# Performance work log

Measured on AMD Instinct MI355X. Metric: run time of the kernel, lower is better.

The kernel has to match this reference:

```python
import jax, jax.numpy as jnp
import numpy as np

B = 2
H = 256; Wd = 256; C = 128; S = 16        # image dims, channels, split_size
G = (H // S) * (Wd // S)                  # 256 heads (spatial groups)
N = S * S                                 # 256 patches per head
CI = C // 2                               # 64 channels per branch (gmlp input)
EI = 6                                    # inner gMLP expansion (MabGmlpBlock default e)
F1 = CI * EI                              # 384 = LocallyConnected expansion width
HF = F1 // 2                              # 192 = u/v split width
EPS = 1e-3                                # keras LayerNormalization default epsilon


def layer_norm(x, g, b):
    m = jnp.mean(x, axis=-1, keepdims=True)
    v = jnp.var(x, axis=-1, keepdims=True)
    return (x - m) * jax.lax.rsqrt(v + EPS) * g + b


def make_blocks(x):
    # 'B (H b1) (W b2) C -> B (H W) (b1 b2) C'
    b_, _, _, c_ = x.shape
    x = x.reshape(b_, H // S, S, Wd // S, S, c_)
    return x.transpose(0, 1, 3, 2, 4, 5).reshape(b_, G, N, c_)


def recon_blocks(x):
    # 'B (H W) (b1 b2) C -> B (H b1) (W b2) C'
    b_, _, _, c_ = x.shape
    x = x.reshape(b_, H // S, Wd // S, S, S, c_)
    return x.transpose(0, 1, 3, 2, 4, 5).reshape(b_, H, Wd, c_)


def recon_grids(x):
    # 'B (H W) (d1 d2) C -> B (d1 H) (d2 W) C'
    b_, _, _, c_ = x.shape
    x = x.reshape(b_, H // S, Wd // S, S, S, c_)
    return x.transpose(0, 3, 1, 4, 2, 5).reshape(b_, H, Wd, c_)


def gmlp(x, ln2_g, ln2_b, W1, b1, ln3_g, ln3_b, Wsgu, bsgu, W2, b2):
    # x: [B, G, N, CI]; all heads share weights -> batched einsum over (B, G)
    y = layer_norm(x, ln2_g, ln2_b)
    # LocallyConnected1D kernel_size=1: per-patch distinct weight [N, CI, F1]
    y = jax.nn.gelu(jnp.einsum('bgnc,ncf->bgnf', y, W1) + b1, approximate=False)
    u, v = jnp.split(y, 2, axis=-1)                      # [B,G,N,HF] each
    u = layer_norm(u, ln3_g, ln3_b)
    u = jnp.swapaxes(u, -1, -2)                          # [B,G,HF,N]
    # spatial gating: per-channel distinct [N->N] mixing, bias init ones
    u = jnp.einsum('bgcn,cnm->bgcm', u, Wsgu) + bsgu
    u = jnp.swapaxes(u, -1, -2)                          # [B,G,N,HF]
    return jnp.einsum('bgnc,ncf->bgnf', u * v, W2) + b2 + x


def setup_inputs() -> dict:
    key = jax.random.key(0)
    ks = jax.random.split(key, 8)
    x = jax.random.normal(ks[0], (B, H, Wd, C), jnp.float32)
    W_proj = jax.random.normal(ks[1], (C, C), jnp.float32) / np.sqrt(C).astype(np.float32)
    b_proj = jnp.zeros((C,), jnp.float32)
    W1 = jax.random.normal(ks[2], (N, CI, F1), jnp.float32) / np.sqrt(CI).astype(np.float32)
    b1 = jnp.zeros((N, F1), jnp.float32)
    Wsgu = jax.random.normal(ks[3], (HF, N, N), jnp.float32) * 0.001  # truncated_normal(0.001) approx
    bsgu = jnp.ones((HF, N), jnp.float32)                             # bias_initializer=ones
    W2 = jax.random.normal(ks[4], (N, HF, CI), jnp.float32) / np.sqrt(HF).astype(np.float32)
    b2 = jnp.zeros((N, CI), jnp.float32)
    return {
        'x': x,
        'ln1_g': jnp.ones((C,), jnp.float32), 'ln1_b': jnp.zeros((C,), jnp.float32),
        'W_proj': W_proj, 'b_proj': b_proj,
        'ln2_g': jnp.ones((CI,), jnp.float32), 'ln2_b': jnp.zeros((CI,), jnp.float32),
        'W1': W1, 'b1': b1,
        'ln3_g': jnp.ones((HF,), jnp.float32), 'ln3_b': jnp.zeros((HF,), jnp.float32),
        'Wsgu': Wsgu, 'bsgu': bsgu,
        'W2': W2, 'b2': b2,
    }


def reference(x, ln1_g, ln1_b, W_proj, b_proj, ln2_g, ln2_b, W1, b1,
              ln3_g, ln3_b, Wsgu, bsgu, W2, b2):
    y = layer_norm(x, ln1_g, ln1_b)
    y = jax.nn.gelu(y @ W_proj + b_proj, approximate=False)   # Dense(c*e), e=1
    local, glob = jnp.split(y, 2, axis=-1)                    # [B,H,W,CI] each
    g_args = (ln2_g, ln2_b, W1, b1, ln3_g, ln3_b, Wsgu, bsgu, W2, b2)
    local = recon_grids(gmlp(make_blocks(local), *g_args))    # multi-axis: block in, grid out
    glob = recon_blocks(gmlp(make_blocks(glob), *g_args))
    out = jnp.concatenate([local, glob], axis=-1) + x
    return out, glob
```

## Files before the change

### kernel.cpp

```cpp
#include <hip/hip_runtime.h>


typedef unsigned int uint_t;
typedef unsigned short us_t;
typedef __attribute__((ext_vector_type(8))) short bf16x8;
typedef __attribute__((ext_vector_type(4))) float f32x4;

#define EPSF 1e-3f

__device__ __forceinline__ float b2f(us_t h){ return __uint_as_float(((uint_t)h) << 16); }
__device__ __forceinline__ float lo2f(uint_t u){ return __uint_as_float(u << 16); }
__device__ __forceinline__ float hi2f(uint_t u){ return __uint_as_float(u & 0xFFFF0000u); }
__device__ __forceinline__ us_t f2b(float f){
  uint_t u = __float_as_uint(f);
  uint_t r = (u + 0x7FFFu + ((u >> 16) & 1u)) >> 16;
  return (us_t)r;
}
__device__ __forceinline__ uint_t pack2(float a, float b){
  return (uint_t)f2b(a) | ((uint_t)f2b(b) << 16);
}
__device__ __forceinline__ float gelu_f(float v){
  return 0.5f*v*(1.f + erff(v*0.7071067811865475f));
}

__global__ __launch_bounds__(256) void wprep(const float* __restrict__ Wsgu,
                                             const float* __restrict__ Wp,
                                             us_t* __restrict__ WT,
                                             us_t* __restrict__ WpT){
  __shared__ __align__(16) us_t ls[128*136];
  int t = threadIdx.x;
  if (blockIdx.x == 768){
    #pragma unroll
    for (int i = 0; i < 16; i++){
      int idx = (i*256 + t)*4;
      int row = idx >> 7, col = idx & 127;
      float4 w = *(const float4*)(Wp + idx);
      ls[(col+0)*136 + row] = f2b(w.x);
      ls[(col+1)*136 + row] = f2b(w.y);
      ls[(col+2)*136 + row] = f2b(w.z);
      ls[(col+3)*136 + row] = f2b(w.w);
    }
    __syncthreads();
    #pragma unroll
    for (int i = 0; i < 8; i++){
      int chunk = i*256 + t;
      int o = chunk >> 4, i0 = (chunk & 15) << 3;
      *(uint4*)(WpT + o*128 + i0) = *(const uint4*)&ls[o*136 + i0];
    }
    return;
  }
  int c = blockIdx.x >> 2, kt = blockIdx.x & 3;
  const float* src = Wsgu + ((size_t)c*256 + kt*64)*256;
  #pragma unroll
  for (int i = 0; i < 16; i++){
    int chunk = i*256 + t;
    int kk = chunk >> 6, mm = (chunk & 63) << 2;
    float4 w = *(const float4*)(src + kk*256 + mm);
    *(uint2*)&ls[kk*264 + mm] = make_uint2(pack2(w.x,w.y), pack2(w.z,w.w));
  }
  __syncthreads();
  #pragma unroll
  for (int i = 0; i < 8; i++){
    int chunk = i*256 + t;
    int m = chunk >> 3, kk0 = (chunk & 7) << 3;
    const us_t* sp = &ls[kk0*264 + m];
    uint4 o;
    o.x = (uint_t)sp[0]     | ((uint_t)sp[264]   << 16);
    o.y = (uint_t)sp[2*264] | ((uint_t)sp[3*264] << 16);
    o.z = (uint_t)sp[4*264] | ((uint_t)sp[5*264] << 16);
    o.w = (uint_t)sp[6*264] | ((uint_t)sp[7*264] << 16);
    *(uint4*)(WT + ((size_t)c*256 + m)*256 + kt*64 + kk0) = o;
  }
}

__global__ __launch_bounds__(256) void k1_ln_proj(
    const float* __restrict__ x, const float* __restrict__ g1, const float* __restrict__ b1l,
    const us_t* __restrict__ WpT, const float* __restrict__ bp, us_t* __restrict__ xin)
{
  __shared__ __align__(16) us_t As[128*136];
  __shared__ __align__(16) us_t Ws[128*136];
  __shared__ float gs[128], bs[128];
  int t = threadIdx.x;
  int p0 = blockIdx.x * 128;
  int lane = t & 63, wv = t >> 6;

  if (t < 128){ gs[t] = g1[t]; bs[t] = b1l[t]; }
  #pragma unroll
  for (int i = 0; i < 8; i++){
    int chunk = i*256 + t;
    int row = chunk >> 4, k0 = (chunk & 15) << 3;
    *(uint4*)&Ws[row*136 + k0] = *(const uint4*)(WpT + row*128 + k0);
  }
  int pl = t >> 1, half = t & 1;
  const float* xr = x + (size_t)(p0 + pl)*128 + half*64;
  float xv[64];
  float s = 0.f, q = 0.f;
  #pragma unroll
  for (int i = 0; i < 16; i++){
    float4 d = *(const float4*)(xr + i*4);
    xv[i*4+0] = d.x; xv[i*4+1] = d.y; xv[i*4+2] = d.z; xv[i*4+3] = d.w;
    s += d.x + d.y + d.z + d.w;
    q += d.x*d.x + d.y*d.y + d.z*d.z + d.w*d.w;
  }
  s += __shfl_xor(s, 1, 64);
  q += __shfl_xor(q, 1, 64);
  float m = s*(1.f/128.f);
  float rstd = rsqrtf(q*(1.f/128.f) - m*m + EPSF);
  __syncthreads();
  {
    int c0 = half << 6;
    us_t* dst = &As[pl*136 + c0];
    #pragma unroll
    for (int jj = 0; jj < 8; jj++){
      float y[8];
      #pragma unroll
      for (int k = 0; k < 8; k++){
        int idx = jj*8 + k;
        y[k] = (xv[idx] - m)*rstd*gs[c0 + idx] + bs[c0 + idx];
      }
      uint4 o;
      o.x = pack2(y[0], y[1]);
      o.y = pack2(y[2], y[3]);
      o.z = pack2(y[4], y[5]);
      o.w = pack2(y[6], y[7]);
      *(uint4*)&dst[jj*8] = o;
    }
  }
  __syncthreads();
  int wm0 = (wv >> 1) * 64, wn0 = (wv & 1) * 64;
  int fr = lane & 15, fq = lane >> 4;
  f32x4 acc[4][4] = {};
  #pragma unroll
  for (int sstep = 0; sstep < 4; sstep++){
    int kb = sstep*32 + fq*8;
    bf16x8 a[4], b[4];
    #pragma unroll
    for (int mi = 0; mi < 4; mi++)
      a[mi] = *(const bf16x8*)&Ws[(wm0 + mi*16 + fr)*136 + kb];
    #pragma unroll
    for (int ni = 0; ni < 4; ni++)
      b[ni] = *(const bf16x8*)&As[(wn0 + ni*16 + fr)*136 + kb];
    #pragma unroll
    for (int mi = 0; mi < 4; mi++)
      #pragma unroll
      for (int ni = 0; ni < 4; ni++)
        acc[mi][ni] = __builtin_amdgcn_mfma_f32_16x16x32_bf16(a[mi], b[ni], acc[mi][ni], 0, 0, 0);
  }
  #pragma unroll
  for (int mi = 0; mi < 4; mi++){
    int ch0 = wm0 + mi*16 + fq*4;
    float4 bb = *(const float4*)(bp + ch0);
    int branch = ch0 >> 6, c = ch0 & 63;
    #pragma unroll
    for (int ni = 0; ni < 4; ni++){
      int p = p0 + wn0 + ni*16 + fr;
      int b_ = p >> 16, rem = p & 65535, h = rem >> 8, w = rem & 255;
      int g = ((h >> 4) << 4) | (w >> 4);
      int nn = ((h & 15) << 4) | (w & 15);
      float v0 = gelu_f(acc[mi][ni][0] + bb.x);
      float v1 = gelu_f(acc[mi][ni][1] + bb.y);
      float v2 = gelu_f(acc[mi][ni][2] + bb.z);
      float v3 = gelu_f(acc[mi][ni][3] + bb.w);
      size_t row = (size_t)branch*512 + (size_t)b_*256 + g;
      *(uint2*)(xin + (row*256 + nn)*64 + c) = make_uint2(pack2(v0,v1), pack2(v2,v3));
    }
  }
}

__global__ __launch_bounds__(256) void k2_e1(
    const us_t* __restrict__ xin,
    const float* __restrict__ g2, const float* __restrict__ b2l,
    const float* __restrict__ W1, const float* __restrict__ b1v,
    const float* __restrict__ g3, const float* __restrict__ b3l,
    us_t* __restrict__ u_ln, us_t* __restrict__ vout, int r_base)
{
  __shared__ __align__(16) us_t Wl[64*384];
  __shared__ __align__(16) float xs2[64*36];
  __shared__ float b1s[384];
  int t = threadIdx.x;
  int n = blockIdx.x >> 2, rt = blockIdx.x & 3;

  const float* wsrc = W1 + (size_t)n*24576;
  #pragma unroll
  for (int i = 0; i < 24; i++){
    int idx = (i*256 + t)*4;
    float4 w = *(const float4*)(wsrc + idx);
    *(uint2*)&Wl[idx] = make_uint2(pack2(w.x,w.y), pack2(w.z,w.w));
  }
  if (t < 96){
    float4 d = *(const float4*)(b1v + n*384 + t*4);
    b1s[t*4+0] = d.x; b1s[t*4+1] = d.y; b1s[t*4+2] = d.z; b1s[t*4+3] = d.w;
  }
  {
    int rr = t >> 3, cc0 = (t & 7) << 3;
    uint4 d = *(const uint4*)(xin + ((size_t)(r_base + rt*32 + rr)*256 + n)*64 + cc0);
    float* dst = &xs2[cc0*36 + rr];
    dst[0]    = lo2f(d.x); dst[36]   = hi2f(d.x);
    dst[2*36] = lo2f(d.y); dst[3*36] = hi2f(d.y);
    dst[4*36] = lo2f(d.z); dst[5*36] = hi2f(d.z);
    dst[6*36] = lo2f(d.w); dst[7*36] = hi2f(d.w);
  }
  __syncthreads();
  {
    int wv = t >> 6, ln = t & 63;
    float gch = g2[ln], bch = b2l[ln];
    for (int k = 0; k < 8; k++){
      int row = wv*8 + k;
      float a = xs2[ln*36 + row];
      float s = a, q = a*a;
      #pragma unroll
      for (int off = 32; off; off >>= 1){ s += __shfl_xor(s, off, 64); q += __shfl_xor(q, off, 64); }
      float m = s*(1.f/64.f);
      float rstd = rsqrtf(q*(1.f/64.f) - m*m + EPSF);
      xs2[ln*36 + row] = (a - m)*rstd*gch + bch;
    }
  }
  __syncthreads();
  int fg = t & 31, rg = t >> 5;
  int f0 = fg*12, r00 = rg*4;
  float acc[4][12] = {};
  #pragma unroll 4
  for (int ci = 0; ci < 64; ci++){
    float4 xv = *(const float4*)&xs2[ci*36 + r00];
    const uint2* wp2 = (const uint2*)&Wl[ci*384 + f0];
    uint2 wa = wp2[0], wb = wp2[1], wc = wp2[2];
    float wf[12];
    wf[0]=lo2f(wa.x); wf[1]=hi2f(wa.x); wf[2]=lo2f(wa.y); wf[3]=hi2f(wa.y);
    wf[4]=lo2f(wb.x); wf[5]=hi2f(wb.x); wf[6]=lo2f(wb.y); wf[7]=hi2f(wb.y);
    wf[8]=lo2f(wc.x); wf[9]=hi2f(wc.x); wf[10]=lo2f(wc.y); wf[11]=hi2f(wc.y);
    float xa[4] = {xv.x, xv.y, xv.z, xv.w};
    #pragma unroll
    for (int i = 0; i < 4; i++)
      #pragma unroll
      for (int j = 0; j < 12; j++)
        acc[i][j] += xa[i]*wf[j];
  }
  bool isu = (fg < 16);
  float s4[4], q4[4];
  #pragma unroll
  for (int i = 0; i < 4; i++){
    float s = 0.f, q = 0.f;
    #pragma unroll
    for (int j = 0; j < 12; j++){
      float yv = gelu_f(acc[i][j] + b1s[f0 + j]);
      acc[i][j] = yv;
      s += yv; q += yv*yv;
    }
    s4[i] = isu ? s : 0.f;
    q4[i] = isu ? q : 0.f;
  }
  #pragma unroll
  for (int i = 0; i < 4; i++){
    float s = s4[i], q = q4[i];
    #pragma unroll
    for (int off = 16; off; off >>= 1){ s += __shfl_xor(s, off, 64); q += __shfl_xor(q, off, 64); }
    float m = s*(1.f/192.f);
    s4[i] = m;
    q4[i] = rsqrtf(q*(1.f/192.f) - m*m + EPSF);
  }
  if (isu){
    float gv[12], bv[12];
    #pragma unroll
    for (int j = 0; j < 12; j++){ gv[j] = g3[f0+j]; bv[j] = b3l[f0+j]; }
    #pragma unroll
    for (int i = 0; i < 4; i++){
      int r = rt*32 + r00 + i;
      float m = s4[i], rstd = q4[i];
      uint2* dst = (uint2*)(u_ln + ((size_t)r*256 + n)*192 + f0);
      uint2 o0, o1, o2;
      o0.x = pack2((acc[i][0]-m)*rstd*gv[0]+bv[0],  (acc[i][1]-m)*rstd*gv[1]+bv[1]);
      o0.y = pack2((acc[i][2]-m)*rstd*gv[2]+bv[2],  (acc[i][3]-m)*rstd*gv[3]+bv[3]);
      o1.x = pack2((acc[i][4]-m)*rstd*gv[4]+bv[4],  (acc[i][5]-m)*rstd*gv[5]+bv[5]);
      o1.y = pack2((acc[i][6]-m)*rstd*gv[6]+bv[6],  (acc[i][7]-m)*rstd*gv[7]+bv[7]);
      o2.x = pack2((acc[i][8]-m)*rstd*gv[8]+bv[8],  (acc[i][9]-m)*rstd*gv[9]+bv[9]);
      o2.y = pack2((acc[i][10]-m)*rstd*gv[10]+bv[10],(acc[i][11]-m)*rstd*gv[11]+bv[11]);
      dst[0] = o0; dst[1] = o1; dst[2] = o2;
    }
  } else {
    int fv0 = f0 - 192;
    #pragma unroll
    for (int i = 0; i < 4; i++){
      int r = rt*32 + r00 + i;
      uint2* dst = (uint2*)(vout + ((size_t)r*256 + n)*192 + fv0);
      uint2 o0, o1, o2;
      o0.x = pack2(acc[i][0], acc[i][1]);  o0.y = pack2(acc[i][2], acc[i][3]);
      o1.x = pack2(acc[i][4], acc[i][5]);  o1.y = pack2(acc[i][6], acc[i][7]);
      o2.x = pack2(acc[i][8], acc[i][9]);  o2.y = pack2(acc[i][10], acc[i][11]);
      dst[0] = o0; dst[1] = o1; dst[2] = o2;
    }
  }
}

__global__ __launch_bounds__(256) void t1_transpose(const us_t* __restrict__ u_ln, us_t* __restrict__ uT){
  __shared__ us_t ls[128*194];
  int t = threadIdx.x;
  int r = blockIdx.x >> 1, n0 = (blockIdx.x & 1) << 7;
  #pragma unroll
  for (int i = 0; i < 12; i++){
    int chunk = i*256 + t;
    int nn = chunk/24, c0 = (chunk - nn*24)*8;
    uint4 d = *(const uint4*)(u_ln + ((size_t)r*256 + n0 + nn)*192 + c0);
    us_t* dst = &ls[nn*194 + c0];
    dst[0] = (us_t)d.x; dst[1] = (us_t)(d.x>>16);
    dst[2] = (us_t)d.y; dst[3] = (us_t)(d.y>>16);
    dst[4] = (us_t)d.z; dst[5] = (us_t)(d.z>>16);
    dst[6] = (us_t)d.w; dst[7] = (us_t)(d.w>>16);
  }
  __syncthreads();
  #pragma unroll
  for (int i = 0; i < 12; i++){
    int chunk = i*256 + t;
    int c = chunk >> 4, nn0 = (chunk & 15) << 3;
    const us_t* sp = &ls[nn0*194 + c];
    uint4 o;
    o.x = (uint_t)sp[0]     | ((uint_t)sp[194]   << 16);
    o.y = (uint_t)sp[2*194] | ((uint_t)sp[3*194] << 16);
    o.z = (uint_t)sp[4*194] | ((uint_t)sp[5*194] << 16);
    o.w = (uint_t)sp[6*194] | ((uint_t)sp[7*194] << 16);
    *(uint4*)(uT + ((size_t)c*128 + r)*256 + n0 + nn0) = o;
  }
}

__global__ __launch_bounds__(256) void k3_sgu_mfma(
    const us_t* __restrict__ uT, const us_t* __restrict__ WT,
    const float* __restrict__ bsgu, us_t* __restrict__ sT)
{
  __shared__ __align__(16) us_t As[128*72];
  __shared__ __align__(16) us_t Bs[128*72];
  int t = threadIdx.x;
  int c = blockIdx.x >> 1, mt = blockIdx.x & 1;
  int lane = t & 63, wv = t >> 6;
  int wr0 = (wv >> 1) * 64, wm0 = (wv & 1) * 64;
  int fr = lane & 15, fq = lane >> 4;
  f32x4 acc[4][4] = {};

  const us_t* aSrc = uT + (size_t)c*128*256;
  const us_t* bSrc = WT + ((size_t)(c*256 + mt*128))*256;

  for (int ks = 0; ks < 256; ks += 64){
    #pragma unroll
    for (int i = 0; i < 4; i++){
      int chunk = i*256 + t;
      int rr = chunk >> 3, kk = (chunk & 7) << 3;
      *(uint4*)&As[rr*72 + kk] = *(const uint4*)(aSrc + rr*256 + ks + kk);
      *(uint4*)&Bs[rr*72 + kk] = *(const uint4*)(bSrc + rr*256 + ks + kk);
    }
    __syncthreads();
    #pragma unroll
    for (int s = 0; s < 2; s++){
      int kb = s*32 + fq*8;
      bf16x8 a[4], b[4];
      #pragma unroll
      for (int mi = 0; mi < 4; mi++)
        a[mi] = *(const bf16x8*)&As[(wr0 + mi*16 + fr)*72 + kb];
      #pragma unroll
      for (int ni = 0; ni < 4; ni++)
        b[ni] = *(const bf16x8*)&Bs[(wm0 + ni*16 + fr)*72 + kb];
      #pragma unroll
      for (int mi = 0; mi < 4; mi++)
        #pragma unroll
        for (int ni = 0; ni < 4; ni++)
          acc[mi][ni] = __builtin_amdgcn_mfma_f32_16x16x32_bf16(a[mi], b[ni], acc[mi][ni], 0, 0, 0);
    }
    __syncthreads();
  }
  float bsv[4];
  #pragma unroll
  for (int ni = 0; ni < 4; ni++)
    bsv[ni] = bsgu[c*256 + mt*128 + wm0 + ni*16 + fr];
  #pragma unroll
  for (int mi = 0; mi < 4; mi++){
    #pragma unroll
    for (int i = 0; i < 4; i++){
      int r = wr0 + mi*16 + fq*4 + i;
      us_t* dst = sT + ((size_t)c*128 + r)*256 + mt*128 + wm0 + fr;
      #pragma unroll
      for (int ni = 0; ni < 4; ni++)
        dst[ni*16] = f2b(acc[mi][ni][i] + bsv[ni]);
    }
  }
}

__global__ __launch_bounds__(256) void t2_mul(
    const us_t* __restrict__ sT, const us_t* __restrict__ v, us_t* __restrict__ tout)
{
  __shared__ us_t ls[192*130];
  int t = threadIdx.x;
  int r = blockIdx.x >> 1, m0 = (blockIdx.x & 1) << 7;
  #pragma unroll
  for (int i = 0; i < 12; i++){
    int chunk = i*256 + t;
    int c = chunk >> 4, mm0 = (chunk & 15) << 3;
    uint4 d = *(const uint4*)(sT + ((size_t)c*128 + r)*256 + m0 + mm0);
    us_t* dst = &ls[c*130 + mm0];
    dst[0] = (us_t)d.x; dst[1] = (us_t)(d.x>>16);
    dst[2] = (us_t)d.y; dst[3] = (us_t)(d.y>>16);
    dst[4] = (us_t)d.z; dst[5] = (us_t)(d.z>>16);
    dst[6] = (us_t)d.w; dst[7] = (us_t)(d.w>>16);
  }
  __syncthreads();
  #pragma unroll
  for (int i = 0; i < 12; i++){
    int chunk = i*256 + t;
    int mm = chunk/24, c0 = (chunk - mm*24)*8;
    size_t gidx = ((size_t)r*256 + m0 + mm)*192 + c0;
    uint4 vv = *(const uint4*)(v + gidx);
    const us_t* sp = &ls[c0*130 + mm];
    uint4 o;
    o.x = pack2(b2f(sp[0])*lo2f(vv.x),     b2f(sp[130])*hi2f(vv.x));
    o.y = pack2(b2f(sp[2*130])*lo2f(vv.y), b2f(sp[3*130])*hi2f(vv.y));
    o.z = pack2(b2f(sp[4*130])*lo2f(vv.z), b2f(sp[5*130])*hi2f(vv.z));
    o.w = pack2(b2f(sp[6*130])*lo2f(vv.w), b2f(sp[7*130])*hi2f(vv.w));
    *(uint4*)(tout + gidx) = o;
  }
}

__global__ __launch_bounds__(256) void k4_out(
    const us_t* __restrict__ tbuf, const float* __restrict__ W2,
    const float* __restrict__ b2v, const us_t* __restrict__ xin,
    const float* __restrict__ x, float* __restrict__ out0, float* __restrict__ out1,
    int r_base)
{
  __shared__ __align__(16) us_t W2s[192*64];
  __shared__ __align__(16) us_t ts[192*68];
  int t = threadIdx.x;
  int n = blockIdx.x >> 1, rt = blockIdx.x & 1;
  const float* wsrc = W2 + (size_t)n*12288;
  #pragma unroll
  for (int i = 0; i < 12; i++){
    int idx = (i*256 + t)*4;
    float4 w = *(const float4*)(wsrc + idx);
    *(uint2*)&W2s[idx] = make_uint2(pack2(w.x,w.y), pack2(w.z,w.w));
  }
  #pragma unroll
  for (int i = 0; i < 6; i++){
    int chunk = i*256 + t;
    int rr = chunk/24, ff0 = (chunk - rr*24)*8;
    uint4 d = *(const uint4*)(tbuf + ((size_t)(rt*64 + rr)*256 + n)*192 + ff0);
    us_t* dst = &ts[ff0*68 + rr];
    dst[0]    = (us_t)d.x; dst[68]   = (us_t)(d.x>>16);
    dst[2*68] = (us_t)d.y; dst[3*68] = (us_t)(d.y>>16);
    dst[4*68] = (us_t)d.z; dst[5*68] = (us_t)(d.z>>16);
    dst[6*68] = (us_t)d.w; dst[7*68] = (us_t)(d.w>>16);
  }
  __syncthreads();
  int cg = t & 15, rg = t >> 4;
  int c0 = cg*4, rr0 = rg*4;
  float acc[4][4] = {};
  #pragma unroll 4
  for (int f = 0; f < 192; f++){
    uint2 au = *(const uint2*)&ts[f*68 + rr0];
    uint2 wu = *(const uint2*)&W2s[f*64 + c0];
    float a0 = lo2f(au.x), a1 = hi2f(au.x), a2 = lo2f(au.y), a3 = hi2f(au.y);
    float w0 = lo2f(wu.x), w1 = hi2f(wu.x), w2 = lo2f(wu.y), w3 = hi2f(wu.y);
    acc[0][0] += a0*w0; acc[0][1] += a0*w1; acc[0][2] += a0*w2; acc[0][3] += a0*w3;
    acc[1][0] += a1*w0; acc[1][1] += a1*w1; acc[1][2] += a1*w2; acc[1][3] += a1*w3;
    acc[2][0] += a2*w0; acc[2][1] += a2*w1; acc[2][2] += a2*w2; acc[2][3] += a2*w3;
    acc[3][0] += a3*w0; acc[3][1] += a3*w1; acc[3][2] += a3*w2; acc[3][3] += a3*w3;
  }
  float4 bb = *(const float4*)(b2v + n*64 + c0);
  #pragma unroll
  for (int i = 0; i < 4; i++){
    int rl = rt*64 + rr0 + i;
    int r = r_base + rl;
    int branch = r >> 9, bidx = (r >> 8) & 1, g = r & 255;
    uint2 xi = *(const uint2*)(xin + ((size_t)r*256 + n)*64 + c0);
    float v0 = acc[i][0] + bb.x + lo2f(xi.x);
    float v1 = acc[i][1] + bb.y + hi2f(xi.x);
    float v2 = acc[i][2] + bb.z + lo2f(xi.y);
    float v3 = acc[i][3] + bb.w + hi2f(xi.y);
    int h, w;
    if (branch == 0){ h = ((n >> 4) << 4) | (g >> 4); w = ((n & 15) << 4) | (g & 15); }
    else            { h = ((g >> 4) << 4) | (n >> 4); w = ((g & 15) << 4) | (n & 15); }
    size_t base = (size_t)(bidx*256 + h)*256 + w;
    size_t o0idx = base*128 + (branch << 6) + c0;
    float4 xr = *(const float4*)(x + o0idx);
    *(float4*)(out0 + o0idx) = make_float4(v0 + xr.x, v1 + xr.y, v2 + xr.z, v3 + xr.w);
    if (branch){
      *(float4*)(out1 + base*64 + c0) = make_float4(v0, v1, v2, v3);
    }
  }
}

extern "C" void kernel_launch(void* const* d_in, const int* in_sizes, int n_in,
                              void* d_out, int out_size, void* d_ws, size_t ws_size,
                              hipStream_t stream)
{
  (void)in_sizes; (void)n_in; (void)out_size; (void)ws_size;
  const float* x    = (const float*)d_in[0];
  const float* g1   = (const float*)d_in[1];
  const float* b1l  = (const float*)d_in[2];
  const float* Wp   = (const float*)d_in[3];
  const float* bp   = (const float*)d_in[4];
  const float* g2   = (const float*)d_in[5];
  const float* b2l  = (const float*)d_in[6];
  const float* W1   = (const float*)d_in[7];
  const float* b1v  = (const float*)d_in[8];
  const float* g3   = (const float*)d_in[9];
  const float* b3l  = (const float*)d_in[10];
  const float* Wsgu = (const float*)d_in[11];
  const float* bsgu = (const float*)d_in[12];
  const float* W2   = (const float*)d_in[13];
  const float* b2v  = (const float*)d_in[14];

  float* out0 = (float*)d_out;
  float* out1 = out0 + (size_t)2*256*256*128;

  us_t* ws   = (us_t*)d_ws;
  us_t* xin  = ws;
  us_t* bufA = ws + 16777216;
  us_t* bufV = bufA + 6291456;
  us_t* bufB = bufV + 6291456;
  us_t* WT   = bufB + 6291456;
  us_t* WpT  = WT + 12582912;

  wprep      <<<dim3(769),  dim3(256), 0, stream>>>(Wsgu, Wp, WT, WpT);
  k1_ln_proj <<<dim3(1024), dim3(256), 0, stream>>>(x, g1, b1l, WpT, bp, xin);
  for (int chunk = 0; chunk < 8; ++chunk){
    int r_base = chunk * 128;
    k2_e1       <<<dim3(1024), dim3(256), 0, stream>>>(xin, g2, b2l, W1, b1v, g3, b3l, bufA, bufV, r_base);
    t1_transpose<<<dim3(256),  dim3(256), 0, stream>>>(bufA, bufB);
    k3_sgu_mfma <<<dim3(384),  dim3(256), 0, stream>>>(bufB, WT, bsgu, bufA);
    t2_mul      <<<dim3(256),  dim3(256), 0, stream>>>(bufA, bufV, bufB);
    k4_out      <<<dim3(512),  dim3(256), 0, stream>>>(bufB, W2, b2v, xin, x, out0, out1, r_base);
  }
}
```

Baseline: 1.178 ms.

## Rewrite k2_e1 expansion GEMM with bf16 MFMA and split u/v across blocks

Replaces the scalar FMA loop in the per-patch LocallyConnected expansion kernel with bf16 MFMA 16x16x32 instructions. Each block now handles all 128 rows for one patch and one half (u or v) of the output features. The layer norm over the input is done in registers per row pair instead of via a transposed shared buffer. This trades scalar ALU work for matrix-core throughput and halves per-block weight staging, but the epilogue now writes 2-byte scattered stores strided by 16 elements, which may hurt store coalescing.

```diff
diff --git a/kernel.cpp b/kernel.cpp
--- a/kernel.cpp
+++ b/kernel.cpp
@@ -174,119 +174,137 @@
     const float* __restrict__ g3, const float* __restrict__ b3l,
     us_t* __restrict__ u_ln, us_t* __restrict__ vout, int r_base)
 {
-  __shared__ __align__(16) us_t Wl[64*384];
-  __shared__ __align__(16) float xs2[64*36];
-  __shared__ float b1s[384];
-  int t = threadIdx.x;
-  int n = blockIdx.x >> 2, rt = blockIdx.x & 3;
-
-  const float* wsrc = W1 + (size_t)n*24576;
-  #pragma unroll
-  for (int i = 0; i < 24; i++){
-    int idx = (i*256 + t)*4;
-    float4 w = *(const float4*)(wsrc + idx);
-    *(uint2*)&Wl[idx] = make_uint2(pack2(w.x,w.y), pack2(w.z,w.w));
-  }
-  if (t < 96){
-    float4 d = *(const float4*)(b1v + n*384 + t*4);
-    b1s[t*4+0] = d.x; b1s[t*4+1] = d.y; b1s[t*4+2] = d.z; b1s[t*4+3] = d.w;
-  }
+  __shared__ __align__(16) us_t Bs[192*72];
+  __shared__ __align__(16) us_t As[128*72];
+  __shared__ __align__(16) float b1s[192];
+  __shared__ __align__(16) float g3s[192];
+  __shared__ __align__(16) float b3s[192];
+  __shared__ __align__(16) float g2s[64];
+  __shared__ __align__(16) float b2s[64];
+  int t = threadIdx.x;
+  int n = blockIdx.x >> 1, uv = blockIdx.x & 1;
+  int lane = t & 63, wv = t >> 6;
+  int fr = lane & 15, fq = lane >> 4;
+
+  const float* wsrc = W1 + (size_t)n*24576 + uv*192;
+  #pragma unroll
+  for (int i = 0; i < 12; i++){
+    int chunk = i*256 + t;
+    int ci = chunk & 63, fb = chunk >> 6;
+    float4 w = *(const float4*)(wsrc + ci*384 + fb*4);
+    us_t* dst = &Bs[(fb*4)*72 + ci];
+    dst[0]   = f2b(w.x);
+    dst[72]  = f2b(w.y);
+    dst[144] = f2b(w.z);
+    dst[216] = f2b(w.w);
+  }
+  if (t < 48)        *(float4*)&b1s[t*4]       = *(const float4*)(b1v + n*384 + uv*192 + t*4);
+  else if (t < 96)   *(float4*)&g3s[(t-48)*4]  = *(const float4*)(g3  + (t-48)*4);
+  else if (t < 144)  *(float4*)&b3s[(t-96)*4]  = *(const float4*)(b3l + (t-96)*4);
+  else if (t < 160)  *(float4*)&g2s[(t-144)*4] = *(const float4*)(g2  + (t-144)*4);
+  else if (t < 176)  *(float4*)&b2s[(t-160)*4] = *(const float4*)(b2l + (t-160)*4);
+
+  int rr = t >> 1, half = t & 1;
+  const us_t* xsrc = xin + ((size_t)(r_base + rr)*256 + n)*64 + half*32;
+  uint4 d0 = *(const uint4*)(xsrc);
+  uint4 d1 = *(const uint4*)(xsrc + 8);
+  uint4 d2 = *(const uint4*)(xsrc + 16);
+  uint4 d3 = *(const uint4*)(xsrc + 24);
+  float xv[32];
   {
-    int rr = t >> 3, cc0 = (t & 7) << 3;
-    uint4 d = *(const uint4*)(xin + ((size_t)(r_base + rt*32 + rr)*256 + n)*64 + cc0);
-    float* dst = &xs2[cc0*36 + rr];
-    dst[0]    = lo2f(d.x); dst[36]   = hi2f(d.x);
-    dst[2*36] = lo2f(d.y); dst[3*36] = hi2f(d.y);
-    dst[4*36] = lo2f(d.z); dst[5*36] = hi2f(d.z);
-    dst[6*36] = lo2f(d.w); dst[7*36] = hi2f(d.w);
-  }
+    uint4 dd[4] = {d0, d1, d2, d3};
+    #pragma unroll
+    for (int j = 0; j < 4; j++){
+      xv[j*8+0]=lo2f(dd[j].x); xv[j*8+1]=hi2f(dd[j].x);
+      xv[j*8+2]=lo2f(dd[j].y); xv[j*8+3]=hi2f(dd[j].y);
+      xv[j*8+4]=lo2f(dd[j].z); xv[j*8+5]=hi2f(dd[j].z);
+      xv[j*8+6]=lo2f(dd[j].w); xv[j*8+7]=hi2f(dd[j].w);
+    }
+  }
+  float s = 0.f, q = 0.f;
+  #pragma unroll
+  for (int j = 0; j < 32; j++){ s += xv[j]; q += xv[j]*xv[j]; }
+  s += __shfl_xor(s, 1, 64);
+  q += __shfl_xor(q, 1, 64);
+  float m = s*(1.f/64.f);
+  float rstd = rsqrtf(q*(1.f/64.f) - m*m + EPSF);
   __syncthreads();
   {
-    int wv = t >> 6, ln = t & 63;
-    float gch = g2[ln], bch = b2l[ln];
-    for (int k = 0; k < 8; k++){
-      int row = wv*8 + k;
-      float a = xs2[ln*36 + row];
-      float s = a, q = a*a;
-      #pragma unroll
-      for (int off = 32; off; off >>= 1){ s += __shfl_xor(s, off, 64); q += __shfl_xor(q, off, 64); }
-      float m = s*(1.f/64.f);
-      float rstd = rsqrtf(q*(1.f/64.f) - m*m + EPSF);
-      xs2[ln*36 + row] = (a - m)*rstd*gch + bch;
-    }
-  }
-  __syncthreads();
-  int fg = t & 31, rg = t >> 5;
-  int f0 = fg*12, r00 = rg*4;
-  float acc[4][12] = {};
-  #pragma unroll 4
-  for (int ci = 0; ci < 64; ci++){
-    float4 xv = *(const float4*)&xs2[ci*36 + r00];
-    const uint2* wp2 = (const uint2*)&Wl[ci*384 + f0];
-    uint2 wa = wp2[0], wb = wp2[1], wc = wp2[2];
-    float wf[12];
-    wf[0]=lo2f(wa.x); wf[1]=hi2f(wa.x); wf[2]=lo2f(wa.y); wf[3]=hi2f(wa.y);
-    wf[4]=lo2f(wb.x); wf[5]=hi2f(wb.x); wf[6]=lo2f(wb.y); wf[7]=hi2f(wb.y);
-    wf[8]=lo2f(wc.x); wf[9]=hi2f(wc.x); wf[10]=lo2f(wc.y); wf[11]=hi2f(wc.y);
-    float xa[4] = {xv.x, xv.y, xv.z, xv.w};
-    #pragma unroll
-    for (int i = 0; i < 4; i++)
-      #pragma unroll
-      for (int j = 0; j < 12; j++)
-        acc[i][j] += xa[i]*wf[j];
-  }
-  bool isu = (fg < 16);
-  float s4[4], q4[4];
-  #pragma unroll
-  for (int i = 0; i < 4; i++){
-    float s = 0.f, q = 0.f;
-    #pragma unroll
-    for (int j = 0; j < 12; j++){
-      float yv = gelu_f(acc[i][j] + b1s[f0 + j]);
-      acc[i][j] = yv;
-      s += yv; q += yv*yv;
-    }
-    s4[i] = isu ? s : 0.f;
-    q4[i] = isu ? q : 0.f;
-  }
-  #pragma unroll
-  for (int i = 0; i < 4; i++){
-    float s = s4[i], q = q4[i];
-    #pragma unroll
-    for (int off = 16; off; off >>= 1){ s += __shfl_xor(s, off, 64); q += __shfl_xor(q, off, 64); }
-    float m = s*(1.f/192.f);
-    s4[i] = m;
-    q4[i] = rsqrtf(q*(1.f/192.f) - m*m + EPSF);
-  }
-  if (isu){
-    float gv[12], bv[12];
-    #pragma unroll
-    for (int j = 0; j < 12; j++){ gv[j] = g3[f0+j]; bv[j] = b3l[f0+j]; }
-    #pragma unroll
-    for (int i = 0; i < 4; i++){
-      int r = rt*32 + r00 + i;
-      float m = s4[i], rstd = q4[i];
-      uint2* dst = (uint2*)(u_ln + ((size_t)r*256 + n)*192 + f0);
-      uint2 o0, o1, o2;
-      o0.x = pack2((acc[i][0]-m)*rstd*gv[0]+bv[0],  (acc[i][1]-m)*rstd*gv[1]+bv[1]);
-      o0.y = pack2((acc[i][2]-m)*rstd*gv[2]+bv[2],  (acc[i][3]-m)*rstd*gv[3]+bv[3]);
-      o1.x = pack2((acc[i][4]-m)*rstd*gv[4]+bv[4],  (acc[i][5]-m)*rstd*gv[5]+bv[5]);
-      o1.y = pack2((acc[i][6]-m)*rstd*gv[6]+bv[6],  (acc[i][7]-m)*rstd*gv[7]+bv[7]);
-      o2.x = pack2((acc[i][8]-m)*rstd*gv[8]+bv[8],  (acc[i][9]-m)*rstd*gv[9]+bv[9]);
-      o2.y = pack2((acc[i][10]-m)*rstd*gv[10]+bv[10],(acc[i][11]-m)*rstd*gv[11]+bv[11]);
-      dst[0] = o0; dst[1] = o1; dst[2] = o2;
+    int cb = half*32;
+    us_t* dst = &As[rr*72 + cb];
+    #pragma unroll
+    for (int jj = 0; jj < 4; jj++){
+      float y[8];
+      #pragma unroll
+      for (int k = 0; k < 8; k++){
+        int idx = cb + jj*8 + k;
+        y[k] = (xv[jj*8+k] - m)*rstd*g2s[idx] + b2s[idx];
+      }
+      uint4 o;
+      o.x = pack2(y[0], y[1]);
+      o.y = pack2(y[2], y[3]);
+      o.z = pack2(y[4], y[5]);
+      o.w = pack2(y[6], y[7]);
+      *(uint4*)&dst[jj*8] = o;
+    }
+  }
+  __syncthreads();
+
+  int wr0 = wv*32;
+  f32x4 acc[2][12] = {};
+  #pragma unroll
+  for (int ks = 0; ks < 2; ks++){
+    int kb = ks*32 + fq*8;
+    bf16x8 a0 = *(const bf16x8*)&As[(wr0 + fr)*72 + kb];
+    bf16x8 a1 = *(const bf16x8*)&As[(wr0 + 16 + fr)*72 + kb];
+    #pragma unroll
+    for (int ni = 0; ni < 12; ni++){
+      bf16x8 b = *(const bf16x8*)&Bs[(ni*16 + fr)*72 + kb];
+      acc[0][ni] = __builtin_amdgcn_mfma_f32_16x16x32_bf16(a0, b, acc[0][ni], 0, 0, 0);
+      acc[1][ni] = __builtin_amdgcn_mfma_f32_16x16x32_bf16(a1, b, acc[1][ni], 0, 0, 0);
+    }
+  }
+
+  float bsv[12];
+  #pragma unroll
+  for (int ni = 0; ni < 12; ni++) bsv[ni] = b1s[ni*16 + fr];
+  if (uv == 0){
+    float g3v[12], b3v[12];
+    #pragma unroll
+    for (int ni = 0; ni < 12; ni++){ g3v[ni] = g3s[ni*16+fr]; b3v[ni] = b3s[ni*16+fr]; }
+    #pragma unroll
+    for (int mi = 0; mi < 2; mi++){
+      #pragma unroll
+      for (int i = 0; i < 4; i++){
+        int r = wr0 + mi*16 + fq*4 + i;
+        float y[12];
+        float ss = 0.f, qq = 0.f;
+        #pragma unroll
+        for (int ni = 0; ni < 12; ni++){
+          float yv = gelu_f(acc[mi][ni][i] + bsv[ni]);
+          y[ni] = yv; ss += yv; qq += yv*yv;
+        }
+        #pragma unroll
+        for (int off = 8; off; off >>= 1){ ss += __shfl_xor(ss, off, 64); qq += __shfl_xor(qq, off, 64); }
+        float mm = ss*(1.f/192.f);
+        float rs = rsqrtf(qq*(1.f/192.f) - mm*mm + EPSF);
+        us_t* dst = u_ln + ((size_t)r*256 + n)*192 + fr;
+        #pragma unroll
+        for (int ni = 0; ni < 12; ni++)
+          dst[ni*16] = f2b((y[ni]-mm)*rs*g3v[ni] + b3v[ni]);
+      }
     }
   } else {
-    int fv0 = f0 - 192;
-    #pragma unroll
-    for (int i = 0; i < 4; i++){
-      int r = rt*32 + r00 + i;
-      uint2* dst = (uint2*)(vout + ((size_t)r*256 + n)*192 + fv0);
-      uint2 o0, o1, o2;
-      o0.x = pack2(acc[i][0], acc[i][1]);  o0.y = pack2(acc[i][2], acc[i][3]);
-      o1.x = pack2(acc[i][4], acc[i][5]);  o1.y = pack2(acc[i][6], acc[i][7]);
-      o2.x = pack2(acc[i][8], acc[i][9]);  o2.y = pack2(acc[i][10], acc[i][11]);
-      dst[0] = o0; dst[1] = o1; dst[2] = o2;
+    #pragma unroll
+    for (int mi = 0; mi < 2; mi++){
+      #pragma unroll
+      for (int i = 0; i < 4; i++){
+        int r = wr0 + mi*16 + fq*4 + i;
+        us_t* dst = vout + ((size_t)r*256 + n)*192 + fr;
+        #pragma unroll
+        for (int ni = 0; ni < 12; ni++)
+          dst[ni*16] = f2b(gelu_f(acc[mi][ni][i] + bsv[ni]));
+      }
     }
   }
 }
@@ -518,7 +536,7 @@
   k1_ln_proj <<<dim3(1024), dim3(256), 0, stream>>>(x, g1, b1l, WpT, bp, xin);
   for (int chunk = 0; chunk < 8; ++chunk){
     int r_base = chunk * 128;
-    k2_e1       <<<dim3(1024), dim3(256), 0, stream>>>(xin, g2, b2l, W1, b1v, g3, b3l, bufA, bufV, r_base);
+    k2_e1       <<<dim3(512),  dim3(256), 0, stream>>>(xin, g2, b2l, W1, b1v, g3, b3l, bufA, bufV, r_base);
     t1_transpose<<<dim3(256),  dim3(256), 0, stream>>>(bufA, bufB);
     k3_sgu_mfma <<<dim3(384),  dim3(256), 0, stream>>>(bufB, WT, bsgu, bufA);
     t2_mul      <<<dim3(256),  dim3(256), 0, stream>>>(bufA, bufV, bufB);
```

Measured after the change: 1.375 ms. 1.17x slower.
